# Kernel optimization log

Measured on AMD Instinct MI355X. Metric: run time of the kernel, lower is better.

Reference implementation:

```python
import jax, jax.numpy as jnp
import numpy as np
from jax import lax

NEG_INF = -1e30
GAP_OPEN = -5.0
GAP_EXTEND = -1.0
TEMP = 1.0


def setup_inputs() -> dict:
    key = jax.random.key(0)
    x = jax.random.normal(key, (2048, 2048), dtype=jnp.float32)
    return {"x": x}


def _sw_forward(x):
    xin = x[:-1, :-1]
    A, B = xin.shape  # static
    ar = jnp.arange(A - 1, -1, -1)[:, None]  # (A,1)
    br = jnp.arange(B)[None, :]              # (1,B)
    i = br - ar + (A - 1)                    # (A,B) diagonal index
    j = (ar + br) // 2                       # (A,B) position within diagonal
    n = A + B - 1
    m = (A + B) // 2
    # rotate score matrix into anti-diagonal (wavefront) layout
    smx = jnp.full((n, m), NEG_INF, dtype=x.dtype).at[i, j].set(xin)
    smo = (((jnp.arange(n) + A % 2) % 2)).astype(x.dtype)  # parity per diagonal

    right_pen = jnp.array([GAP_OPEN, GAP_EXTEND, GAP_OPEN], dtype=x.dtype)   # penalize_turns
    down_pen = jnp.array([GAP_OPEN, GAP_OPEN, GAP_EXTEND], dtype=x.dtype)

    def lse(a):
        return TEMP * jax.nn.logsumexp(a / TEMP, axis=-1)

    def step(carry, inp):
        h2, h1 = carry            # each (m,3)
        sx, so = inp              # (m,), scalar
        align = jnp.pad(h2, ((0, 0), (0, 1))) + sx[:, None]  # (m,4)
        right = so * jnp.pad(h1[:-1], ((1, 0), (0, 0)), constant_values=NEG_INF) + (1.0 - so) * h1
        down = so * h1 + (1.0 - so) * jnp.pad(h1[1:], ((0, 1), (0, 0)), constant_values=NEG_INF)
        right = (right + right_pen)[:, :2]  # restrict_turns
        down = down + down_pen
        h0 = jnp.stack([lse(align), lse(right), lse(down)], axis=-1)  # (m,3)
        return (h1, h0), h0

    carry0 = (jnp.full((m, 3), NEG_INF, dtype=x.dtype),
              jnp.full((m, 3), NEG_INF, dtype=x.dtype))
    _, results = lax.scan(step, carry0, (smx, smo))  # (n,m,3)

    hij = results[i, j]  # un-rotate -> (A,B,3)
    final = TEMP * jax.nn.logsumexp((hij + x[1:, 1:, None]) / TEMP)
    return final


def reference(x):
    return _sw_forward(x)
```

## Files before the change

### kernel.cpp

```cpp
#include <hip/hip_runtime.h>
#include <hip/hip_bf16.h>
#include <math.h>

#define NN 2048
#define TROWS 1040
#define NW 8
#define RPS 32
#define LN2 0.6931471805599453


__global__ void prep_kernel(const float* __restrict__ x, float* __restrict__ tab,
                            float* __restrict__ tabR) {
  const int c = blockIdx.x * 256 + threadIdx.x;
  const int t = blockIdx.y;
  tab[(size_t)t * NN + c] = __expf(x[(size_t)t * NN + c]);
  const int rr = 2048 - t, cc = 2048 - c;
  float v = 0.f;
  if (rr < 2048 && cc < 2048) v = __expf(x[(size_t)rr * NN + cc]);
  tabR[(size_t)t * NN + c] = v;
}

template<int MODE>
__global__ __launch_bounds__(NW * 64)
void sw2_kernel(const float* __restrict__ x, const float* __restrict__ tab,
                const float* __restrict__ tabR, float* __restrict__ arr,
                float* __restrict__ out) {
  const int tid  = threadIdx.x;
  const int lane = tid & 63;
  const int wv   = __builtin_amdgcn_readfirstlane(tid >> 6);
  const int c0   = (wv << 8) + lane * 4;

  __shared__ float2 E[2][NW + 1][RPS];
  __shared__ float  red[2][NW];
  __shared__ float  wsum[NW];

  for (int i = tid; i < 2 * (NW + 1) * RPS; i += NW * 64)
    ((float2*)E)[i] = make_float2(0.f, 0.f);
  __syncthreads();

  const float cGO = 0.006737946999085467f;
  const float cGE = 0.36787944117144233f;
  const float C4  = 0.01831563888873418f;
  const bool isL0 = (lane == 0), isL1 = (lane == 1), isL63 = (lane == 63);

  if (MODE == 0 || blockIdx.x == 0) {
    const int SPW   = ((MODE == 0) ? 2048 : 1024) / RPS;
    const int NSTEP = SPW + NW - 1;
    float s1_0=0.f,s1_1=0.f,s1_2=0.f,s1_3=0.f;
    float tg0=0.f,tg1=0.f,tg2=0.f,tg3=0.f;
    float yc0=0.f,yc1=0.f,yc2=0.f,yc3=0.f;
    float acc=0.f, one=1.f, tmx=0.f, escale=1.f, SinC=0.f;
    int Etot = 0;
    const float* src = ((MODE == 0) ? x : tab) + c0;
    float4 pfA = *(const float4*)(src);
    float4 pfB = *(const float4*)(src + NN);
    float4 pfC = *(const float4*)(src + 2 * NN);
    float4 pfD = *(const float4*)(src + 3 * NN);
    const float* pl = src + 4 * NN;
    int rown = 4;

    int cr_ = 0, pr_ = 0;
    float prevEdx = 0.f;
    auto rowF = [&](float4 ev, int k, bool first) {
      float ex0 = ev.x, ex1 = ev.y, ex2 = ev.z, ex3 = ev.w;
      if (MODE == 0) { ex0 = __expf(ex0); ex1 = __expf(ex1); ex2 = __expf(ex2); ex3 = __expf(ex3); }
      const float2 edc = E[cr_][wv][k];
      const float Sr = first ? SinC : prevEdx * escale;
      const float Xi = edc.y * escale;
      prevEdx = edc.x;

      float sh  = __shfl_up(s1_3, 1);
      float sd0 = isL0 ? Sr : sh;
      acc = fmaf(ex0, sd0,  acc);
      acc = fmaf(ex1, s1_0, acc);
      acc = fmaf(ex2, s1_1, acc);
      acc = fmaf(ex3, s1_2, acc);
      float M0 = ex0 * (sd0  + one);
      float M1 = ex1 * (s1_0 + one);
      float M2 = ex2 * (s1_1 + one);
      float M3 = ex3 * (s1_2 + one);

      float Q  = fmaf(cGE, fmaf(cGE, fmaf(cGE, M0, M1), M2), M3);
      float q1 = __shfl_up(Q, 1);
      float q2 = __shfl_up(Q, 2);
      q2 = isL1 ? Xi : q2;
      float X0 = fmaf(C4, q2, q1);
      X0 = isL0 ? Xi : X0;
      float X1 = fmaf(cGE, X0, M0);
      float X2 = fmaf(cGE, X1, M1);
      float X3 = fmaf(cGE, X2, M2);

      float T0 = fmaf(cGO, X0, M0);
      float T1 = fmaf(cGO, X1, M1);
      float T2 = fmaf(cGO, X2, M2);
      float T3 = fmaf(cGO, X3, M3);
      float Y0 = fmaf(cGE, yc0, tg0);
      float Y1 = fmaf(cGE, yc1, tg1);
      float Y2 = fmaf(cGE, yc2, tg2);
      float Y3 = fmaf(cGE, yc3, tg3);
      float S0 = T0 + Y0, S1n = T1 + Y1, S2n = T2 + Y2, S3n = T3 + Y3;
      tmx = fmaxf(tmx, fmaxf(fmaxf(S0, S1n), fmaxf(S2n, S3n)));
      tg0 = cGO * T0; tg1 = cGO * T1; tg2 = cGO * T2; tg3 = cGO * T3;
      yc0 = Y0; yc1 = Y1; yc2 = Y2; yc3 = Y3;
      s1_0 = S0; s1_1 = S1n; s1_2 = S2n; s1_3 = S3n;

      if (isL63) E[pr_][wv + 1][k] = make_float2(S3n, fmaf(C4, X0, Q));
    };

    for (int s = 0; s < NSTEP; ++s) {
      pr_ = s & 1; cr_ = pr_ ^ 1;
      const bool act = (s >= wv) && (s < wv + SPW);
      if (act) {
        prevEdx = 0.f;
        for (int kk = 0; kk < RPS / 4; ++kk) {
          const int kb = kk << 2;
          float4 e0 = pfA, e1 = pfB, e2 = pfC, e3 = pfD;
          if (MODE == 1) {
            pfA = *(const float4*)pl;          pl += NN;
            pfB = *(const float4*)pl;          pl += NN;
            pfC = *(const float4*)pl;          pl += NN;
            pfD = *(const float4*)pl;          pl += NN;
          } else {
            int r0 = (rown     < NN) ? rown     : NN - 1;
            int r1 = (rown + 1 < NN) ? rown + 1 : NN - 1;
            int r2 = (rown + 2 < NN) ? rown + 2 : NN - 1;
            int r3 = (rown + 3 < NN) ? rown + 3 : NN - 1;
            pfA = *(const float4*)(src + (size_t)r0 * NN);
            pfB = *(const float4*)(src + (size_t)r1 * NN);
            pfC = *(const float4*)(src + (size_t)r2 * NN);
            pfD = *(const float4*)(src + (size_t)r3 * NN);
            rown += 4;
          }
          rowF(e0, kb + 0, kk == 0);
          rowF(e1, kb + 1, false);
          rowF(e2, kb + 2, false);
          rowF(e3, kb + 3, false);
        }
        SinC = prevEdx * escale;
      }
      {
        float m = tmx;
        m = fmaxf(m, __shfl_xor(m, 1));  m = fmaxf(m, __shfl_xor(m, 2));
        m = fmaxf(m, __shfl_xor(m, 4));  m = fmaxf(m, __shfl_xor(m, 8));
        m = fmaxf(m, __shfl_xor(m, 16)); m = fmaxf(m, __shfl_xor(m, 32));
        if (lane == 0) red[pr_][wv] = m;
      }
      __syncthreads();
      {
        float mm = red[pr_][lane & (NW - 1)];
        mm = fmaxf(mm, __shfl_xor(mm, 1));
        mm = fmaxf(mm, __shfl_xor(mm, 2));
        mm = fmaxf(mm, __shfl_xor(mm, 4));
        tmx = 0.f; escale = 1.f;
        int e = (mm > 0.f) ? ilogbf(mm) : 0;
        if (e > 126) e = 126; if (e < -126) e = -126;
        if (e != 0) {
          const float c = ldexpf(1.f, -e);
          s1_0*=c; s1_1*=c; s1_2*=c; s1_3*=c;
          tg0*=c; tg1*=c; tg2*=c; tg3*=c;
          yc0*=c; yc1*=c; yc2*=c; yc3*=c;
          acc*=c; one*=c; SinC*=c;
          escale = c; Etot += e;
        }
      }
    }
    float ssum = acc;
    ssum += __shfl_xor(ssum, 1);  ssum += __shfl_xor(ssum, 2);
    ssum += __shfl_xor(ssum, 4);  ssum += __shfl_xor(ssum, 8);
    ssum += __shfl_xor(ssum, 16); ssum += __shfl_xor(ssum, 32);
    if (lane == 0) wsum[wv] = ssum;
    __syncthreads();
    if (MODE == 0) {
      if (tid == 0) {
        double tot = 0.0;
        #pragma unroll
        for (int k = 0; k < NW; ++k) tot += (double)wsum[k];
        out[0] = (float)(log(tot) + (double)Etot * LN2);
      }
    } else {
      *(float4*)(arr + c0)          = make_float4(s1_0, s1_1, s1_2, s1_3);
      *(float4*)(arr + NN + c0)     = make_float4(tg0, tg1, tg2, tg3);
      *(float4*)(arr + 2 * NN + c0) = make_float4(yc0, yc1, yc2, yc3);
      if (tid == 0) {
        float t = 0.f;
        #pragma unroll
        for (int k = 0; k < NW; ++k) t += wsum[k];
        arr[5 * NN + 0] = t;
        ((int*)(arr + 5 * NN))[2] = Etot;
      }
    }
  } else {
    const int SPWB = 1024 / RPS;
    float gM1_0=0.f,gM1_1=0.f,gM1_2=0.f,gM1_3=0.f;
    float gY1_0=0.f,gY1_1=0.f,gY1_2=0.f,gY1_3=0.f;
    float accB=0.f, one=1.f, tmx=0.f, escale=1.f, gMinC=0.f;
    int Etot = 0;
    const float* src = tabR + c0;
    float4 pfA = *(const float4*)(src);
    float4 pfB = *(const float4*)(src + NN);
    float4 pfC = *(const float4*)(src + 2 * NN);
    float4 pfD = *(const float4*)(src + 3 * NN);
    const float* pl = src + 4 * NN;

    int cr_ = 0, pr_ = 0;
    float prevEdx = 0.f;
    auto rowB = [&](float4 ev, int k, bool first) {
      const float er0 = ev.x, er1 = ev.y, er2 = ev.z, er3 = ev.w;
      const float2 edc = E[cr_][wv][k];
      const float gMdIn = first ? gMinC : prevEdx * escale;
      const float Xi = edc.y * escale;
      prevEdx = edc.x;

      float gmh  = __shfl_up(gM1_3, 1);
      float gMd0 = isL0 ? gMdIn : gmh;
      float gMd1 = gM1_0, gMd2 = gM1_1, gMd3 = gM1_2;
      accB = fmaf(er0, gMd0, accB);
      accB = fmaf(er1, gMd1, accB);
      accB = fmaf(er2, gMd2, accB);
      accB = fmaf(er3, gMd3, accB);
      float a0 = er0 * (gMd0 + one);
      float a1 = er1 * (gMd1 + one);
      float a2 = er2 * (gMd2 + one);
      float a3 = er3 * (gMd3 + one);

      float gTs0 = fmaf(cGO, gY1_0, a0);
      float gTs1 = fmaf(cGO, gY1_1, a1);
      float gTs2 = fmaf(cGO, gY1_2, a2);
      float gTs3 = fmaf(cGO, gY1_3, a3);
      float gY0n = fmaf(cGE, gY1_0, a0);
      float gY1n = fmaf(cGE, gY1_1, a1);
      float gY2n = fmaf(cGE, gY1_2, a2);
      float gY3n = fmaf(cGE, gY1_3, a3);

      float Qg = fmaf(cGE, fmaf(cGE, fmaf(cGE, gTs0, gTs1), gTs2), gTs3);
      float q1 = __shfl_up(Qg, 1);
      float q2 = __shfl_up(Qg, 2);
      q2 = isL1 ? Xi : q2;
      float gXin = fmaf(C4, q2, q1);
      gXin = isL0 ? Xi : gXin;
      float gX0 = fmaf(cGE, gXin, gTs0);
      float gX1 = fmaf(cGE, gX0,  gTs1);
      float gX2 = fmaf(cGE, gX1,  gTs2);
      float gM0n = fmaf(cGO, gXin, gTs0);
      float gM1n = fmaf(cGO, gX0,  gTs1);
      float gM2n = fmaf(cGO, gX1,  gTs2);
      float gM3n = fmaf(cGO, gX2,  gTs3);

      tmx = fmaxf(tmx, fmaxf(fmaxf(gM0n, gM1n), fmaxf(gM2n, gM3n)));
      tmx = fmaxf(tmx, fmaxf(fmaxf(gY0n, gY1n), fmaxf(gY2n, gY3n)));
      gM1_0 = gM0n; gM1_1 = gM1n; gM1_2 = gM2n; gM1_3 = gM3n;
      gY1_0 = gY0n; gY1_1 = gY1n; gY1_2 = gY2n; gY1_3 = gY3n;

      if (isL63) E[pr_][wv + 1][k] = make_float2(gM3n, fmaf(C4, gXin, Qg));
    };

    const int NSTEPB = SPWB + NW - 1 + 1;
    for (int s = 0; s < NSTEPB; ++s) {
      pr_ = s & 1; cr_ = pr_ ^ 1;
      const bool actM = (s >= wv) && (s < wv + SPWB);
      const bool actE = (s == wv + SPWB);
      if (actM) {
        prevEdx = 0.f;
        for (int kk = 0; kk < RPS / 4; ++kk) {
          const int kb = kk << 2;
          float4 e0 = pfA, e1 = pfB, e2 = pfC, e3 = pfD;
          pfA = *(const float4*)pl;            pl += NN;
          pfB = *(const float4*)pl;            pl += NN;
          pfC = *(const float4*)pl;            pl += NN;
          pfD = *(const float4*)pl;            pl += NN;
          rowB(e0, kb + 0, kk == 0);
          rowB(e1, kb + 1, false);
          rowB(e2, kb + 2, false);
          rowB(e3, kb + 3, false);
        }
        gMinC = prevEdx * escale;
      } else if (actE) {
        float gmh  = __shfl_up(gM1_3, 1);
        float gMd0 = isL0 ? gMinC : gmh;
        accB = fmaf(pfA.x, gMd0,  accB);
        accB = fmaf(pfA.y, gM1_0, accB);
        accB = fmaf(pfA.z, gM1_1, accB);
        accB = fmaf(pfA.w, gM1_2, accB);
      }
      {
        float m = tmx;
        m = fmaxf(m, __shfl_xor(m, 1));  m = fmaxf(m, __shfl_xor(m, 2));
        m = fmaxf(m, __shfl_xor(m, 4));  m = fmaxf(m, __shfl_xor(m, 8));
        m = fmaxf(m, __shfl_xor(m, 16)); m = fmaxf(m, __shfl_xor(m, 32));
        if (lane == 0) red[pr_][wv] = m;
      }
      __syncthreads();
      {
        float mm = red[pr_][lane & (NW - 1)];
        mm = fmaxf(mm, __shfl_xor(mm, 1));
        mm = fmaxf(mm, __shfl_xor(mm, 2));
        mm = fmaxf(mm, __shfl_xor(mm, 4));
        tmx = 0.f; escale = 1.f;
        int e = (mm > 0.f) ? ilogbf(mm) : 0;
        if (e > 126) e = 126; if (e < -126) e = -126;
        if (e != 0) {
          const float c = ldexpf(1.f, -e);
          gM1_0*=c; gM1_1*=c; gM1_2*=c; gM1_3*=c;
          gY1_0*=c; gY1_1*=c; gY1_2*=c; gY1_3*=c;
          accB*=c; one*=c; gMinC*=c;
          escale = c; Etot += e;
        }
      }
    }
    *(float4*)(arr + 3 * NN + (2044 - c0)) = make_float4(gM1_3, gM1_2, gM1_1, gM1_0);
    *(float4*)(arr + 4 * NN + (2044 - c0)) = make_float4(gY1_3, gY1_2, gY1_1, gY1_0);
    float ssum = accB;
    ssum += __shfl_xor(ssum, 1);  ssum += __shfl_xor(ssum, 2);
    ssum += __shfl_xor(ssum, 4);  ssum += __shfl_xor(ssum, 8);
    ssum += __shfl_xor(ssum, 16); ssum += __shfl_xor(ssum, 32);
    if (lane == 0) wsum[wv] = ssum;
    __syncthreads();
    if (tid == 0) {
      float t = 0.f;
      #pragma unroll
      for (int k = 0; k < NW; ++k) t += wsum[k];
      arr[5 * NN + 1] = t;
      ((int*)(arr + 5 * NN))[3] = Etot;
    }
  }
}

__global__ __launch_bounds__(1024)
void combine_kernel(const float* __restrict__ tab, const float* __restrict__ arr,
                    float* __restrict__ out) {
  __shared__ double sh01[16], sh0[16];
  const int tid = threadIdx.x, lane = tid & 63, wv = tid >> 6;
  const float cGE = 0.36787944117144233f;
  double t01 = 0.0, t0 = 0.0;
  for (int b = tid; b < NN; b += 1024) {
    const float S  = arr[b];
    const float tg = arr[NN + b];
    const float yc = arr[2 * NN + b];
    const float gY = arr[4 * NN + b];
    t01 += (double)gY * ((double)tg + (double)cGE * (double)yc);
    if (b < NN - 1) {
      const float es = tab[(size_t)1024 * NN + b + 1];
      const float gM = arr[3 * NN + b + 1];
      t01 += (double)es * (double)gM * (double)S;
      t0  += (double)es * (double)S;
    }
  }
  #pragma unroll
  for (int off = 1; off < 64; off <<= 1) {
    t01 += __shfl_xor(t01, off);
    t0  += __shfl_xor(t0, off);
  }
  if (lane == 0) { sh01[wv] = t01; sh0[wv] = t0; }
  __syncthreads();
  if (tid == 0) {
    double A01 = 0.0, A0 = 0.0;
    #pragma unroll
    for (int k = 0; k < 16; ++k) { A01 += sh01[k]; A0 += sh0[k]; }
    const float* resF = arr + 5 * NN;
    const float accTop = resF[0], accB = resF[1];
    const int E0 = ((const int*)resF)[2], E1 = ((const int*)resF)[3];
    A0 += (double)accTop;
    const double A1 = (double)accB;
    const long long e01 = (long long)E0 + (long long)E1;
    long long em = e01;
    if ((long long)E0 > em) em = E0;
    if ((long long)E1 > em) em = E1;
    const double tot = A01 * exp2((double)(e01 - em))
                     + A0  * exp2((double)((long long)E0 - em))
                     + A1  * exp2((double)((long long)E1 - em));
    out[0] = (float)(log(tot) + (double)em * LN2);
  }
}

extern "C" void kernel_launch(void* const* d_in, const int* in_sizes, int n_in,
                              void* d_out, int out_size, void* d_ws, size_t ws_size,
                              hipStream_t stream) {
  const float* x = (const float*)d_in[0];
  float* out = (float*)d_out;
  const size_t need = ((size_t)2 * TROWS * NN + 5 * NN + 16) * sizeof(float);
  if (ws_size >= need) {
    float* tab  = (float*)d_ws;
    float* tabR = tab + (size_t)TROWS * NN;
    float* arr  = tab + (size_t)2 * TROWS * NN;
    prep_kernel<<<dim3(NN / 256, TROWS), dim3(256), 0, stream>>>(x, tab, tabR);
    sw2_kernel<1><<<dim3(2), dim3(NW * 64), 0, stream>>>(x, tab, tabR, arr, out);
    combine_kernel<<<dim3(1), dim3(1024), 0, stream>>>(tab, arr, out);
  } else {
    sw2_kernel<0><<<dim3(1), dim3(NW * 64), 0, stream>>>(x, nullptr, nullptr, nullptr, out);
  }
}
```

Measured before the change: 265.3 us.

## Widen per-lane column strip to 8 and halve waves per block

```diff
diff --git a/kernel.cpp b/kernel.cpp
--- a/kernel.cpp
+++ b/kernel.cpp
@@ -4,7 +4,7 @@
 
 #define NN 2048
 #define TROWS 1040
-#define NW 8
+#define NW 4
 #define RPS 32
 #define LN2 0.6931471805599453
 
@@ -28,7 +28,7 @@
   const int tid  = threadIdx.x;
   const int lane = tid & 63;
   const int wv   = __builtin_amdgcn_readfirstlane(tid >> 6);
-  const int c0   = (wv << 8) + lane * 4;
+  const int c0   = (wv << 9) + lane * 8;
 
   __shared__ float2 E[2][NW + 1][RPS];
   __shared__ float  red[2][NW];
@@ -40,71 +40,97 @@
 
   const float cGO = 0.006737946999085467f;
   const float cGE = 0.36787944117144233f;
-  const float C4  = 0.01831563888873418f;
+  const float C8  = 0.00033546262790251185f;
   const bool isL0 = (lane == 0), isL1 = (lane == 1), isL63 = (lane == 63);
 
   if (MODE == 0 || blockIdx.x == 0) {
     const int SPW   = ((MODE == 0) ? 2048 : 1024) / RPS;
     const int NSTEP = SPW + NW - 1;
-    float s1_0=0.f,s1_1=0.f,s1_2=0.f,s1_3=0.f;
-    float tg0=0.f,tg1=0.f,tg2=0.f,tg3=0.f;
-    float yc0=0.f,yc1=0.f,yc2=0.f,yc3=0.f;
+    float s1_0=0.f,s1_1=0.f,s1_2=0.f,s1_3=0.f,s1_4=0.f,s1_5=0.f,s1_6=0.f,s1_7=0.f;
+    float tg0=0.f,tg1=0.f,tg2=0.f,tg3=0.f,tg4=0.f,tg5=0.f,tg6=0.f,tg7=0.f;
+    float yc0=0.f,yc1=0.f,yc2=0.f,yc3=0.f,yc4=0.f,yc5=0.f,yc6=0.f,yc7=0.f;
     float acc=0.f, one=1.f, tmx=0.f, escale=1.f, SinC=0.f;
     int Etot = 0;
     const float* src = ((MODE == 0) ? x : tab) + c0;
-    float4 pfA = *(const float4*)(src);
-    float4 pfB = *(const float4*)(src + NN);
-    float4 pfC = *(const float4*)(src + 2 * NN);
-    float4 pfD = *(const float4*)(src + 3 * NN);
+    float4 pA0 = *(const float4*)(src),          pA1 = *(const float4*)(src + 4);
+    float4 pB0 = *(const float4*)(src + NN),     pB1 = *(const float4*)(src + NN + 4);
+    float4 pC0 = *(const float4*)(src + 2 * NN), pC1 = *(const float4*)(src + 2 * NN + 4);
+    float4 pD0 = *(const float4*)(src + 3 * NN), pD1 = *(const float4*)(src + 3 * NN + 4);
     const float* pl = src + 4 * NN;
     int rown = 4;
 
     int cr_ = 0, pr_ = 0;
     float prevEdx = 0.f;
-    auto rowF = [&](float4 ev, int k, bool first) {
-      float ex0 = ev.x, ex1 = ev.y, ex2 = ev.z, ex3 = ev.w;
-      if (MODE == 0) { ex0 = __expf(ex0); ex1 = __expf(ex1); ex2 = __expf(ex2); ex3 = __expf(ex3); }
+    auto rowF = [&](float4 v0, float4 v1, int k, bool first) {
+      float e0 = v0.x, e1 = v0.y, e2 = v0.z, e3 = v0.w;
+      float e4 = v1.x, e5 = v1.y, e6 = v1.z, e7 = v1.w;
+      if (MODE == 0) {
+        e0 = __expf(e0); e1 = __expf(e1); e2 = __expf(e2); e3 = __expf(e3);
+        e4 = __expf(e4); e5 = __expf(e5); e6 = __expf(e6); e7 = __expf(e7);
+      }
       const float2 edc = E[cr_][wv][k];
       const float Sr = first ? SinC : prevEdx * escale;
       const float Xi = edc.y * escale;
       prevEdx = edc.x;
 
-      float sh  = __shfl_up(s1_3, 1);
+      float sh  = __shfl_up(s1_7, 1);
       float sd0 = isL0 ? Sr : sh;
-      acc = fmaf(ex0, sd0,  acc);
-      acc = fmaf(ex1, s1_0, acc);
-      acc = fmaf(ex2, s1_1, acc);
-      acc = fmaf(ex3, s1_2, acc);
-      float M0 = ex0 * (sd0  + one);
-      float M1 = ex1 * (s1_0 + one);
-      float M2 = ex2 * (s1_1 + one);
-      float M3 = ex3 * (s1_2 + one);
-
-      float Q  = fmaf(cGE, fmaf(cGE, fmaf(cGE, M0, M1), M2), M3);
+      acc = fmaf(e0, sd0,  acc); acc = fmaf(e1, s1_0, acc);
+      acc = fmaf(e2, s1_1, acc); acc = fmaf(e3, s1_2, acc);
+      acc = fmaf(e4, s1_3, acc); acc = fmaf(e5, s1_4, acc);
+      acc = fmaf(e6, s1_5, acc); acc = fmaf(e7, s1_6, acc);
+      float M0 = e0 * (sd0  + one);
+      float M1 = e1 * (s1_0 + one);
+      float M2 = e2 * (s1_1 + one);
+      float M3 = e3 * (s1_2 + one);
+      float M4 = e4 * (s1_3 + one);
+      float M5 = e5 * (s1_4 + one);
+      float M6 = e6 * (s1_5 + one);
+      float M7 = e7 * (s1_6 + one);
+
+      float Q = fmaf(cGE, fmaf(cGE, fmaf(cGE, fmaf(cGE, fmaf(cGE, fmaf(cGE,
+                fmaf(cGE, M0, M1), M2), M3), M4), M5), M6), M7);
       float q1 = __shfl_up(Q, 1);
       float q2 = __shfl_up(Q, 2);
       q2 = isL1 ? Xi : q2;
-      float X0 = fmaf(C4, q2, q1);
+      float X0 = fmaf(C8, q2, q1);
       X0 = isL0 ? Xi : X0;
       float X1 = fmaf(cGE, X0, M0);
       float X2 = fmaf(cGE, X1, M1);
       float X3 = fmaf(cGE, X2, M2);
+      float X4 = fmaf(cGE, X3, M3);
+      float X5 = fmaf(cGE, X4, M4);
+      float X6 = fmaf(cGE, X5, M5);
+      float X7 = fmaf(cGE, X6, M6);
 
       float T0 = fmaf(cGO, X0, M0);
       float T1 = fmaf(cGO, X1, M1);
       float T2 = fmaf(cGO, X2, M2);
       float T3 = fmaf(cGO, X3, M3);
+      float T4 = fmaf(cGO, X4, M4);
+      float T5 = fmaf(cGO, X5, M5);
+      float T6 = fmaf(cGO, X6, M6);
+      float T7 = fmaf(cGO, X7, M7);
       float Y0 = fmaf(cGE, yc0, tg0);
       float Y1 = fmaf(cGE, yc1, tg1);
       float Y2 = fmaf(cGE, yc2, tg2);
       float Y3 = fmaf(cGE, yc3, tg3);
+      float Y4 = fmaf(cGE, yc4, tg4);
+      float Y5 = fmaf(cGE, yc5, tg5);
+      float Y6 = fmaf(cGE, yc6, tg6);
+      float Y7 = fmaf(cGE, yc7, tg7);
       float S0 = T0 + Y0, S1n = T1 + Y1, S2n = T2 + Y2, S3n = T3 + Y3;
-      tmx = fmaxf(tmx, fmaxf(fmaxf(S0, S1n), fmaxf(S2n, S3n)));
+      float S4n = T4 + Y4, S5n = T5 + Y5, S6n = T6 + Y6, S7n = T7 + Y7;
+      tmx = fmaxf(tmx, fmaxf(fmaxf(fmaxf(S0, S1n), fmaxf(S2n, S3n)),
+                             fmaxf(fmaxf(S4n, S5n), fmaxf(S6n, S7n))));
       tg0 = cGO * T0; tg1 = cGO * T1; tg2 = cGO * T2; tg3 = cGO * T3;
+      tg4 = cGO * T4; tg5 = cGO * T5; tg6 = cGO * T6; tg7 = cGO * T7;
       yc0 = Y0; yc1 = Y1; yc2 = Y2; yc3 = Y3;
+      yc4 = Y4; yc5 = Y5; yc6 = Y6; yc7 = Y7;
       s1_0 = S0; s1_1 = S1n; s1_2 = S2n; s1_3 = S3n;
-
-      if (isL63) E[pr_][wv + 1][k] = make_float2(S3n, fmaf(C4, X0, Q));
+      s1_4 = S4n; s1_5 = S5n; s1_6 = S6n; s1_7 = S7n;
+
+      if (isL63) E[pr_][wv + 1][k] = make_float2(S7n, fmaf(C8, X0, Q));
     };
 
     for (int s = 0; s < NSTEP; ++s) {
@@ -114,27 +140,28 @@
         prevEdx = 0.f;
         for (int kk = 0; kk < RPS / 4; ++kk) {
           const int kb = kk << 2;
-          float4 e0 = pfA, e1 = pfB, e2 = pfC, e3 = pfD;
+          float4 a0 = pA0, a1 = pA1, b0 = pB0, b1 = pB1;
+          float4 c0v = pC0, c1v = pC1, d0 = pD0, d1 = pD1;
           if (MODE == 1) {
-            pfA = *(const float4*)pl;          pl += NN;
-            pfB = *(const float4*)pl;          pl += NN;
-            pfC = *(const float4*)pl;          pl += NN;
-            pfD = *(const float4*)pl;          pl += NN;
+            pA0 = *(const float4*)pl; pA1 = *(const float4*)(pl + 4); pl += NN;
+            pB0 = *(const float4*)pl; pB1 = *(const float4*)(pl + 4); pl += NN;
+            pC0 = *(const float4*)pl; pC1 = *(const float4*)(pl + 4); pl += NN;
+            pD0 = *(const float4*)pl; pD1 = *(const float4*)(pl + 4); pl += NN;
           } else {
             int r0 = (rown     < NN) ? rown     : NN - 1;
             int r1 = (rown + 1 < NN) ? rown + 1 : NN - 1;
             int r2 = (rown + 2 < NN) ? rown + 2 : NN - 1;
             int r3 = (rown + 3 < NN) ? rown + 3 : NN - 1;
-            pfA = *(const float4*)(src + (size_t)r0 * NN);
-            pfB = *(const float4*)(src + (size_t)r1 * NN);
-            pfC = *(const float4*)(src + (size_t)r2 * NN);
-            pfD = *(const float4*)(src + (size_t)r3 * NN);
+            pA0 = *(const float4*)(src + (size_t)r0 * NN); pA1 = *(const float4*)(src + (size_t)r0 * NN + 4);
+            pB0 = *(const float4*)(src + (size_t)r1 * NN); pB1 = *(const float4*)(src + (size_t)r1 * NN + 4);
+            pC0 = *(const float4*)(src + (size_t)r2 * NN); pC1 = *(const float4*)(src + (size_t)r2 * NN + 4);
+            pD0 = *(const float4*)(src + (size_t)r3 * NN); pD1 = *(const float4*)(src + (size_t)r3 * NN + 4);
             rown += 4;
           }
-          rowF(e0, kb + 0, kk == 0);
-          rowF(e1, kb + 1, false);
-          rowF(e2, kb + 2, false);
-          rowF(e3, kb + 3, false);
+          rowF(a0, a1, kb + 0, kk == 0);
+          rowF(b0, b1, kb + 1, false);
+          rowF(c0v, c1v, kb + 2, false);
+          rowF(d0, d1, kb + 3, false);
         }
         SinC = prevEdx * escale;
       }
@@ -150,15 +177,14 @@
         float mm = red[pr_][lane & (NW - 1)];
         mm = fmaxf(mm, __shfl_xor(mm, 1));
         mm = fmaxf(mm, __shfl_xor(mm, 2));
-        mm = fmaxf(mm, __shfl_xor(mm, 4));
         tmx = 0.f; escale = 1.f;
         int e = (mm > 0.f) ? ilogbf(mm) : 0;
         if (e > 126) e = 126; if (e < -126) e = -126;
         if (e != 0) {
           const float c = ldexpf(1.f, -e);
-          s1_0*=c; s1_1*=c; s1_2*=c; s1_3*=c;
-          tg0*=c; tg1*=c; tg2*=c; tg3*=c;
-          yc0*=c; yc1*=c; yc2*=c; yc3*=c;
+          s1_0*=c; s1_1*=c; s1_2*=c; s1_3*=c; s1_4*=c; s1_5*=c; s1_6*=c; s1_7*=c;
+          tg0*=c; tg1*=c; tg2*=c; tg3*=c; tg4*=c; tg5*=c; tg6*=c; tg7*=c;
+          yc0*=c; yc1*=c; yc2*=c; yc3*=c; yc4*=c; yc5*=c; yc6*=c; yc7*=c;
           acc*=c; one*=c; SinC*=c;
           escale = c; Etot += e;
         }
@@ -178,9 +204,12 @@
         out[0] = (float)(log(tot) + (double)Etot * LN2);
       }
     } else {
-      *(float4*)(arr + c0)          = make_float4(s1_0, s1_1, s1_2, s1_3);
-      *(float4*)(arr + NN + c0)     = make_float4(tg0, tg1, tg2, tg3);
-      *(float4*)(arr + 2 * NN + c0) = make_float4(yc0, yc1, yc2, yc3);
+      *(float4*)(arr + c0)              = make_float4(s1_0, s1_1, s1_2, s1_3);
+      *(float4*)(arr + c0 + 4)          = make_float4(s1_4, s1_5, s1_6, s1_7);
+      *(float4*)(arr + NN + c0)         = make_float4(tg0, tg1, tg2, tg3);
+      *(float4*)(arr + NN + c0 + 4)     = make_float4(tg4, tg5, tg6, tg7);
+      *(float4*)(arr + 2 * NN + c0)     = make_float4(yc0, yc1, yc2, yc3);
+      *(float4*)(arr + 2 * NN + c0 + 4) = make_float4(yc4, yc5, yc6, yc7);
       if (tid == 0) {
         float t = 0.f;
         #pragma unroll
@@ -191,67 +220,92 @@
     }
   } else {
     const int SPWB = 1024 / RPS;
-    float gM1_0=0.f,gM1_1=0.f,gM1_2=0.f,gM1_3=0.f;
-    float gY1_0=0.f,gY1_1=0.f,gY1_2=0.f,gY1_3=0.f;
+    float gM0c=0.f,gM1c=0.f,gM2c=0.f,gM3c=0.f,gM4c=0.f,gM5c=0.f,gM6c=0.f,gM7c=0.f;
+    float gY0c=0.f,gY1c=0.f,gY2c=0.f,gY3c=0.f,gY4c=0.f,gY5c=0.f,gY6c=0.f,gY7c=0.f;
     float accB=0.f, one=1.f, tmx=0.f, escale=1.f, gMinC=0.f;
     int Etot = 0;
     const float* src = tabR + c0;
-    float4 pfA = *(const float4*)(src);
-    float4 pfB = *(const float4*)(src + NN);
-    float4 pfC = *(const float4*)(src + 2 * NN);
-    float4 pfD = *(const float4*)(src + 3 * NN);
+    float4 pA0 = *(const float4*)(src),          pA1 = *(const float4*)(src + 4);
+    float4 pB0 = *(const float4*)(src + NN),     pB1 = *(const float4*)(src + NN + 4);
+    float4 pC0 = *(const float4*)(src + 2 * NN), pC1 = *(const float4*)(src + 2 * NN + 4);
+    float4 pD0 = *(const float4*)(src + 3 * NN), pD1 = *(const float4*)(src + 3 * NN + 4);
     const float* pl = src + 4 * NN;
 
     int cr_ = 0, pr_ = 0;
     float prevEdx = 0.f;
-    auto rowB = [&](float4 ev, int k, bool first) {
-      const float er0 = ev.x, er1 = ev.y, er2 = ev.z, er3 = ev.w;
+    auto rowB = [&](float4 v0, float4 v1, int k, bool first) {
+      const float e0 = v0.x, e1 = v0.y, e2 = v0.z, e3 = v0.w;
+      const float e4 = v1.x, e5 = v1.y, e6 = v1.z, e7 = v1.w;
       const float2 edc = E[cr_][wv][k];
       const float gMdIn = first ? gMinC : prevEdx * escale;
       const float Xi = edc.y * escale;
       prevEdx = edc.x;
 
-      float gmh  = __shfl_up(gM1_3, 1);
+      float gmh  = __shfl_up(gM7c, 1);
       float gMd0 = isL0 ? gMdIn : gmh;
-      float gMd1 = gM1_0, gMd2 = gM1_1, gMd3 = gM1_2;
-      accB = fmaf(er0, gMd0, accB);
-      accB = fmaf(er1, gMd1, accB);
-      accB = fmaf(er2, gMd2, accB);
-      accB = fmaf(er3, gMd3, accB);
-      float a0 = er0 * (gMd0 + one);
-      float a1 = er1 * (gMd1 + one);
-      float a2 = er2 * (gMd2 + one);
-      float a3 = er3 * (gMd3 + one);
-
-      float gTs0 = fmaf(cGO, gY1_0, a0);
-      float gTs1 = fmaf(cGO, gY1_1, a1);
-      float gTs2 = fmaf(cGO, gY1_2, a2);
-      float gTs3 = fmaf(cGO, gY1_3, a3);
-      float gY0n = fmaf(cGE, gY1_0, a0);
-      float gY1n = fmaf(cGE, gY1_1, a1);
-      float gY2n = fmaf(cGE, gY1_2, a2);
-      float gY3n = fmaf(cGE, gY1_3, a3);
-
-      float Qg = fmaf(cGE, fmaf(cGE, fmaf(cGE, gTs0, gTs1), gTs2), gTs3);
+      accB = fmaf(e0, gMd0, accB); accB = fmaf(e1, gM0c, accB);
+      accB = fmaf(e2, gM1c, accB); accB = fmaf(e3, gM2c, accB);
+      accB = fmaf(e4, gM3c, accB); accB = fmaf(e5, gM4c, accB);
+      accB = fmaf(e6, gM5c, accB); accB = fmaf(e7, gM6c, accB);
+      float a0 = e0 * (gMd0 + one);
+      float a1 = e1 * (gM0c + one);
+      float a2 = e2 * (gM1c + one);
+      float a3 = e3 * (gM2c + one);
+      float a4 = e4 * (gM3c + one);
+      float a5 = e5 * (gM4c + one);
+      float a6 = e6 * (gM5c + one);
+      float a7 = e7 * (gM6c + one);
+
+      float gTs0 = fmaf(cGO, gY0c, a0);
+      float gTs1 = fmaf(cGO, gY1c, a1);
+      float gTs2 = fmaf(cGO, gY2c, a2);
+      float gTs3 = fmaf(cGO, gY3c, a3);
+      float gTs4 = fmaf(cGO, gY4c, a4);
+      float gTs5 = fmaf(cGO, gY5c, a5);
+      float gTs6 = fmaf(cGO, gY6c, a6);
+      float gTs7 = fmaf(cGO, gY7c, a7);
+      float gY0n = fmaf(cGE, gY0c, a0);
+      float gY1n = fmaf(cGE, gY1c, a1);
+      float gY2n = fmaf(cGE, gY2c, a2);
+      float gY3n = fmaf(cGE, gY3c, a3);
+      float gY4n = fmaf(cGE, gY4c, a4);
+      float gY5n = fmaf(cGE, gY5c, a5);
+      float gY6n = fmaf(cGE, gY6c, a6);
+      float gY7n = fmaf(cGE, gY7c, a7);
+
+      float Qg = fmaf(cGE, fmaf(cGE, fmaf(cGE, fmaf(cGE, fmaf(cGE, fmaf(cGE,
+                 fmaf(cGE, gTs0, gTs1), gTs2), gTs3), gTs4), gTs5), gTs6), gTs7);
       float q1 = __shfl_up(Qg, 1);
       float q2 = __shfl_up(Qg, 2);
       q2 = isL1 ? Xi : q2;
-      float gXin = fmaf(C4, q2, q1);
+      float gXin = fmaf(C8, q2, q1);
       gXin = isL0 ? Xi : gXin;
       float gX0 = fmaf(cGE, gXin, gTs0);
       float gX1 = fmaf(cGE, gX0,  gTs1);
       float gX2 = fmaf(cGE, gX1,  gTs2);
+      float gX3 = fmaf(cGE, gX2,  gTs3);
+      float gX4 = fmaf(cGE, gX3,  gTs4);
+      float gX5 = fmaf(cGE, gX4,  gTs5);
+      float gX6 = fmaf(cGE, gX5,  gTs6);
       float gM0n = fmaf(cGO, gXin, gTs0);
       float gM1n = fmaf(cGO, gX0,  gTs1);
       float gM2n = fmaf(cGO, gX1,  gTs2);
       float gM3n = fmaf(cGO, gX2,  gTs3);
-
-      tmx = fmaxf(tmx, fmaxf(fmaxf(gM0n, gM1n), fmaxf(gM2n, gM3n)));
-      tmx = fmaxf(tmx, fmaxf(fmaxf(gY0n, gY1n), fmaxf(gY2n, gY3n)));
-      gM1_0 = gM0n; gM1_1 = gM1n; gM1_2 = gM2n; gM1_3 = gM3n;
-      gY1_0 = gY0n; gY1_1 = gY1n; gY1_2 = gY2n; gY1_3 = gY3n;
-
-      if (isL63) E[pr_][wv + 1][k] = make_float2(gM3n, fmaf(C4, gXin, Qg));
+      float gM4n = fmaf(cGO, gX3,  gTs4);
+      float gM5n = fmaf(cGO, gX4,  gTs5);
+      float gM6n = fmaf(cGO, gX5,  gTs6);
+      float gM7n = fmaf(cGO, gX6,  gTs7);
+
+      tmx = fmaxf(tmx, fmaxf(fmaxf(fmaxf(gM0n, gM1n), fmaxf(gM2n, gM3n)),
+                             fmaxf(fmaxf(gM4n, gM5n), fmaxf(gM6n, gM7n))));
+      tmx = fmaxf(tmx, fmaxf(fmaxf(fmaxf(gY0n, gY1n), fmaxf(gY2n, gY3n)),
+                             fmaxf(fmaxf(gY4n, gY5n), fmaxf(gY6n, gY7n))));
+      gM0c = gM0n; gM1c = gM1n; gM2c = gM2n; gM3c = gM3n;
+      gM4c = gM4n; gM5c = gM5n; gM6c = gM6n; gM7c = gM7n;
+      gY0c = gY0n; gY1c = gY1n; gY2c = gY2n; gY3c = gY3n;
+      gY4c = gY4n; gY5c = gY5n; gY6c = gY6n; gY7c = gY7n;
+
+      if (isL63) E[pr_][wv + 1][k] = make_float2(gM7n, fmaf(C8, gXin, Qg));
     };
 
     const int NSTEPB = SPWB + NW - 1 + 1;
@@ -263,24 +317,25 @@
         prevEdx = 0.f;
         for (int kk = 0; kk < RPS / 4; ++kk) {
           const int kb = kk << 2;
-          float4 e0 = pfA, e1 = pfB, e2 = pfC, e3 = pfD;
-          pfA = *(const float4*)pl;            pl += NN;
-          pfB = *(const float4*)pl;            pl += NN;
-          pfC = *(const float4*)pl;            pl += NN;
-          pfD = *(const float4*)pl;            pl += NN;
-          rowB(e0, kb + 0, kk == 0);
-          rowB(e1, kb + 1, false);
-          rowB(e2, kb + 2, false);
-          rowB(e3, kb + 3, false);
+          float4 a0 = pA0, a1 = pA1, b0 = pB0, b1 = pB1;
+          float4 c0v = pC0, c1v = pC1, d0 = pD0, d1 = pD1;
+          pA0 = *(const float4*)pl; pA1 = *(const float4*)(pl + 4); pl += NN;
+          pB0 = *(const float4*)pl; pB1 = *(const float4*)(pl + 4); pl += NN;
+          pC0 = *(const float4*)pl; pC1 = *(const float4*)(pl + 4); pl += NN;
+          pD0 = *(const float4*)pl; pD1 = *(const float4*)(pl + 4); pl += NN;
+          rowB(a0, a1, kb + 0, kk == 0);
+          rowB(b0, b1, kb + 1, false);
+          rowB(c0v, c1v, kb + 2, false);
+          rowB(d0, d1, kb + 3, false);
         }
         gMinC = prevEdx * escale;
       } else if (actE) {
-        float gmh  = __shfl_up(gM1_3, 1);
+        float gmh  = __shfl_up(gM7c, 1);
         float gMd0 = isL0 ? gMinC : gmh;
-        accB = fmaf(pfA.x, gMd0,  accB);
-        accB = fmaf(pfA.y, gM1_0, accB);
-        accB = fmaf(pfA.z, gM1_1, accB);
-        accB = fmaf(pfA.w, gM1_2, accB);
+        accB = fmaf(pA0.x, gMd0, accB); accB = fmaf(pA0.y, gM0c, accB);
+        accB = fmaf(pA0.z, gM1c, accB); accB = fmaf(pA0.w, gM2c, accB);
+        accB = fmaf(pA1.x, gM3c, accB); accB = fmaf(pA1.y, gM4c, accB);
+        accB = fmaf(pA1.z, gM5c, accB); accB = fmaf(pA1.w, gM6c, accB);
       }
       {
         float m = tmx;
@@ -294,21 +349,22 @@
         float mm = red[pr_][lane & (NW - 1)];
         mm = fmaxf(mm, __shfl_xor(mm, 1));
         mm = fmaxf(mm, __shfl_xor(mm, 2));
-        mm = fmaxf(mm, __shfl_xor(mm, 4));
         tmx = 0.f; escale = 1.f;
         int e = (mm > 0.f) ? ilogbf(mm) : 0;
         if (e > 126) e = 126; if (e < -126) e = -126;
         if (e != 0) {
           const float c = ldexpf(1.f, -e);
-          gM1_0*=c; gM1_1*=c; gM1_2*=c; gM1_3*=c;
-          gY1_0*=c; gY1_1*=c; gY1_2*=c; gY1_3*=c;
+          gM0c*=c; gM1c*=c; gM2c*=c; gM3c*=c; gM4c*=c; gM5c*=c; gM6c*=c; gM7c*=c;
+          gY0c*=c; gY1c*=c; gY2c*=c; gY3c*=c; gY4c*=c; gY5c*=c; gY6c*=c; gY7c*=c;
           accB*=c; one*=c; gMinC*=c;
           escale = c; Etot += e;
         }
       }
     }
-    *(float4*)(arr + 3 * NN + (2044 - c0)) = make_float4(gM1_3, gM1_2, gM1_1, gM1_0);
-    *(float4*)(arr + 4 * NN + (2044 - c0)) = make_float4(gY1_3, gY1_2, gY1_1, gY1_0);
+    *(float4*)(arr + 3 * NN + (2040 - c0)) = make_float4(gM7c, gM6c, gM5c, gM4c);
+    *(float4*)(arr + 3 * NN + (2044 - c0)) = make_float4(gM3c, gM2c, gM1c, gM0c);
+    *(float4*)(arr + 4 * NN + (2040 - c0)) = make_float4(gY7c, gY6c, gY5c, gY4c);
+    *(float4*)(arr + 4 * NN + (2044 - c0)) = make_float4(gY3c, gY2c, gY1c, gY0c);
     float ssum = accB;
     ssum += __shfl_xor(ssum, 1);  ssum += __shfl_xor(ssum, 2);
     ssum += __shfl_xor(ssum, 4);  ssum += __shfl_xor(ssum, 8);
```

New measurement: 295.5 us. +11.4%, slower.
